# Kernel optimization log

Measured on AMD Instinct MI355X. Metric: run time of the kernel, lower is better.

## Reference

```python
import jax, jax.numpy as jnp
import numpy as np

N, E, L, F, M = 512, 2048, 16, 16, 8
HOPS = 2      # egonet radius (k_hop_subgraph num_hops)
H = 128       # WL hash buckets
N_ITER = 3    # WeisfeilerLehman(n_iter=3)
TAU = 0.1     # soft-relabeling temperature


def setup_inputs():
    key = jax.random.key(0)
    k0, k1, k2, k3, k4, k5 = jax.random.split(key, 6)
    labels = jax.random.randint(k0, (N,), 0, L)
    x = jax.nn.one_hot(labels, L, dtype=jnp.float32)
    edge_index = jax.random.randint(k1, (2, E), 0, N)
    # filter adjacencies, built exactly as in GKernel.__init__:
    # symmetric 0/1 with zero diagonal
    A = jax.random.uniform(k2, (F, M, M))
    A = ((A + jnp.swapaxes(A, -1, -2)) > 1.0).astype(jnp.float32)
    A = A * (1.0 - jnp.eye(M, dtype=jnp.float32))
    Xlab = jax.random.randint(k3, (F, M), 0, L)
    X = jax.nn.one_hot(Xlab, L, dtype=jnp.float32)
    # injective label -> bucket embedding (random distinct buckets)
    E0 = jax.nn.one_hot(jax.random.permutation(k4, H)[:L], H, dtype=jnp.float32)
    # random projection used to hash (own-label, neighbor-multiset) signatures
    Rproj = jax.random.normal(k5, (2 * H, H), dtype=jnp.float32)
    return {"x": x, "edge_index": edge_index, "P": A, "X": X, "E0": E0, "Rproj": Rproj}


def _wl_features(c0, nbr_sum, mask, Rproj):
    # soft Weisfeiler-Lehman subtree features: at each iteration the new
    # node label is a hash of (own label, neighbor-label multiset); the
    # graph feature is the concatenated per-iteration label histograms.
    c = c0 * mask[:, None]                       # [n, H]
    feats = [c.sum(0)]
    for _ in range(N_ITER):
        sig = jnp.concatenate([c, nbr_sum(c)], axis=-1)        # [n, 2H]
        c = jax.nn.softmax((sig @ Rproj) / TAU, axis=-1) * mask[:, None]
        feats.append(c.sum(0))
    return jnp.concatenate(feats)                # [(N_ITER+1)*H]


def _max_comp_mask(A):
    # largest connected component via min-label propagation (max_comp)
    comp = jnp.arange(M, dtype=jnp.float32)
    Ab = A > 0
    for _ in range(M):
        nbr_min = jnp.min(jnp.where(Ab, comp[None, :], 1e9), axis=1)
        comp = jnp.minimum(comp, nbr_min)
    ci = comp.astype(jnp.int32)
    counts = jax.ops.segment_sum(jnp.ones(M, jnp.float32), ci, num_segments=M)
    best = jnp.argmax(counts)
    return (ci == best).astype(jnp.float32)


def reference(x, edge_index, P, X, E0, Rproj):
    # symmetrize edges (egonets / WL kernels are undirected)
    src = jnp.concatenate([edge_index[0], edge_index[1]])
    dst = jnp.concatenate([edge_index[1], edge_index[0]])
    # --- k-hop egonet node masks (compute_egonets) : reach[i, j] = 1 iff
    # node j is within HOPS hops of root i ---
    reach = jnp.eye(N, dtype=jnp.float32)
    for _ in range(HOPS):
        agg = jax.ops.segment_sum(reach[:, src].T, dst, num_segments=N).T
        reach = jnp.clip(reach + agg, 0.0, 1.0)
    c0 = x @ E0                                  # initial bucket labels [N, H]

    def ego_feat(mask):
        emask = (mask[src] * mask[dst])[:, None]
        def nbr(c):
            return jax.ops.segment_sum(c[src] * emask, dst, num_segments=N)
        return _wl_features(c0, nbr, mask, Rproj)

    ego_feats = jax.vmap(ego_feat)(reach)        # [N, (N_ITER+1)*H]

    def filt_feat(Af, Xf):
        mask = _max_comp_mask(Af)
        Am = Af * mask[:, None] * mask[None, :]
        return _wl_features(Xf @ E0, lambda c: Am @ c, mask, Rproj)

    filt_feats = jax.vmap(filt_feat)(P, X)       # [F, (N_ITER+1)*H]

    # normalized WL kernel: k(g1,g2)/sqrt(k(g1,g1) k(g2,g2)); sim.T -> [N, F]
    sim = filt_feats @ ego_feats.T               # [F, N]
    nf = jnp.linalg.norm(filt_feats, axis=-1)
    ng = jnp.linalg.norm(ego_feats, axis=-1)
    sim = sim / (nf[:, None] * ng[None, :] + 1e-12)
    return sim.T
```

## Files before the change

### kernel.cpp

```cpp
#include <hip/hip_runtime.h>
#include <hip/hip_bf16.h>

#define NN 512
#define EE 2048
#define LL 16
#define FF 16
#define MM 8
#define HH 128
#define CAP_ROWS 40960
#define MAXD 32
#define TAU_SCALE 14.426950408889634f

typedef __attribute__((ext_vector_type(8))) short bf16x8;
typedef __attribute__((ext_vector_type(4))) float f32x4;

constexpr size_t OFF_ADJ   = 0;
constexpr size_t SZ_ADJ    = (size_t)NN * 8 * 8;
constexpr size_t OFF_DEG   = OFF_ADJ + SZ_ADJ;
constexpr size_t SZ_DEG    = (size_t)NN * 4;
constexpr size_t OFF_CNT   = OFF_DEG + SZ_DEG;
constexpr size_t SZ_CNT    = (size_t)NN * 4;
constexpr size_t OFF_ROFF  = OFF_CNT + SZ_CNT;
constexpr size_t SZ_ROFF   = (size_t)(NN + 1) * 4 + 12;
constexpr size_t OFF_BUCKN = OFF_ROFF + SZ_ROFF;
constexpr size_t SZ_BUCKN  = (size_t)NN * 4;
constexpr size_t OFF_BUCKF = OFF_BUCKN + SZ_BUCKN;
constexpr size_t SZ_BUCKF  = (size_t)FF * MM * 4;
constexpr size_t OFF_NLST  = ((OFF_BUCKF + SZ_BUCKF + 63) / 64) * 64;
constexpr size_t SZ_NLST   = (size_t)NN * MAXD * 2;
constexpr size_t OFF_CEGO  = OFF_NLST + SZ_NLST;
constexpr size_t SZ_CEGO   = (size_t)CAP_ROWS * 2;
constexpr size_t OFF_NCNT  = OFF_CEGO + SZ_CEGO;
constexpr size_t SZ_NCNT   = (size_t)CAP_ROWS * 2;
constexpr size_t OFF_RBK   = OFF_NCNT + SZ_NCNT;
constexpr size_t SZ_RBK    = (size_t)CAP_ROWS * 2;
constexpr size_t OFF_NBR   = OFF_RBK + SZ_RBK;
constexpr size_t SZ_NBR    = (size_t)CAP_ROWS * MAXD * 2;
constexpr size_t OFF_NBK   = OFF_NBR + SZ_NBR;
constexpr size_t SZ_NBK    = (size_t)CAP_ROWS * MAXD * 2;
constexpr size_t OFF_EGOF  = ((OFF_NBK + SZ_NBK + 63) / 64) * 64;
constexpr size_t SZ_EGOF   = (size_t)NN * 512 * 4;
constexpr size_t OFF_FILTF = OFF_EGOF + SZ_EGOF;
constexpr size_t SZ_FILTF  = (size_t)FF * 512 * 4;
constexpr size_t OFF_FNORM = OFF_FILTF + SZ_FILTF;
constexpr size_t SZ_FNORM  = 64;
constexpr size_t OFF_CA    = ((OFF_FNORM + SZ_FNORM + 255) / 256) * 256;
constexpr size_t SZ_CBUF   = (size_t)CAP_ROWS * HH * 4;
constexpr size_t OFF_CB    = OFF_CA + SZ_CBUF;

__device__ __forceinline__ unsigned f2bfbits(float x) {
    unsigned u = __float_as_uint(x);
    return (u + 0x7fffu + ((u >> 16) & 1u)) >> 16;
}
__device__ __forceinline__ float bf2f(unsigned hb) { return __uint_as_float(hb << 16); }

__global__ __launch_bounds__(256) void k_build(const int* __restrict__ ei,
                                               const float* __restrict__ x,
                                               const float* __restrict__ X,
                                               const float* __restrict__ E0,
                                               int* __restrict__ degN,
                                               unsigned short* __restrict__ nbrLstN,
                                               unsigned long long* __restrict__ adj,
                                               int* __restrict__ buckN,
                                               int* __restrict__ buckF) {
    int idx = blockIdx.x * blockDim.x + threadIdx.x;
    if (idx < EE) {
        int a = ei[idx], b = ei[EE + idx];
        int p = atomicAdd(&degN[a], 1);
        if (p < MAXD) nbrLstN[(size_t)a * MAXD + p] = (unsigned short)b;
        int q = atomicAdd(&degN[b], 1);
        if (q < MAXD) nbrLstN[(size_t)b * MAXD + q] = (unsigned short)a;
        atomicOr(&adj[(size_t)a * 8 + (b >> 6)], 1ull << (b & 63));
        atomicOr(&adj[(size_t)b * 8 + (a >> 6)], 1ull << (a & 63));
    } else if (idx < EE + NN) {
        int i = idx - EE;
        int lab = 0;
        for (int l = 0; l < LL; ++l) if (x[i * LL + l] > 0.5f) lab = l;
        int b = 0;
        for (int h = 0; h < HH; ++h) if (E0[lab * HH + h] > 0.5f) b = h;
        buckN[i] = b;
    } else if (idx < EE + NN + FF * MM) {
        int fm = idx - EE - NN;
        int lab = 0;
        for (int l = 0; l < LL; ++l) if (X[fm * LL + l] > 0.5f) lab = l;
        int b = 0;
        for (int h = 0; h < HH; ++h) if (E0[lab * HH + h] > 0.5f) b = h;
        buckF[fm] = b;
    }
}

__global__ __launch_bounds__(64) void k_reach(const unsigned long long* __restrict__ adj,
                                              unsigned long long* __restrict__ bitsR,
                                              int* __restrict__ count) {
    __shared__ unsigned long long r1[8];
    __shared__ unsigned long long r2[8];
    int i = blockIdx.x, t = threadIdx.x;
    if (t < 8) {
        unsigned long long v = adj[(size_t)i * 8 + t];
        if (t == (i >> 6)) v |= 1ull << (i & 63);
        r1[t] = v;
        r2[t] = v;
    }
    __syncthreads();
    unsigned long long p[8] = {0, 0, 0, 0, 0, 0, 0, 0};
    for (int rep = 0; rep < 8; ++rep) {
        if ((r1[rep] >> t) & 1ull) {
            int j = t + rep * 64;
#pragma unroll
            for (int w = 0; w < 8; ++w) p[w] |= adj[(size_t)j * 8 + w];
        }
    }
#pragma unroll
    for (int w = 0; w < 8; ++w)
        if (p[w]) atomicOr(&r2[w], p[w]);
    __syncthreads();
    if (t < 8) bitsR[(size_t)i * 8 + t] = r2[t];
    if (t == 0) {
        int acc = 0;
        for (int w = 0; w < 8; ++w) acc += __popcll(r2[w]);
        count[i] = acc;
    }
}

__global__ __launch_bounds__(512) void k_scan(const int* __restrict__ in,
                                              int* __restrict__ out) {
    __shared__ int s[NN];
    int t = threadIdx.x;
    s[t] = in[t];
    __syncthreads();
    for (int d = 1; d < NN; d <<= 1) {
        int v = (t >= d) ? s[t - d] : 0;
        __syncthreads();
        s[t] += v;
        __syncthreads();
    }
    out[t + 1] = s[t];
    if (t == 0) out[0] = 0;
}

__global__ __launch_bounds__(64) void k_pack(const unsigned long long* __restrict__ bitsR,
                                             const int* __restrict__ count,
                                             const int* __restrict__ rowOff,
                                             const int* __restrict__ degN,
                                             const unsigned short* __restrict__ nbrLstN,
                                             const int* __restrict__ buckN,
                                             unsigned short* __restrict__ nbrRow,
                                             unsigned short* __restrict__ nbrBuck,
                                             unsigned short* __restrict__ nbrCnt,
                                             unsigned short* __restrict__ rowBuck,
                                             unsigned short* __restrict__ cegoG,
                                             float* __restrict__ egoF) {
    __shared__ unsigned long long bits[8];
    __shared__ int wpre[8];
    __shared__ unsigned short cmap_s[NN];
    __shared__ unsigned short nodes_s[NN];
    __shared__ float f0[HH];
    int i = blockIdx.x, t = threadIdx.x;
    if (t < 8) bits[t] = bitsR[(size_t)i * 8 + t];
    if (t < 64) { f0[t] = 0.0f; f0[t + 64] = 0.0f; }
    __syncthreads();
    if (t == 0) {
        int acc = 0;
        for (int w = 0; w < 8; ++w) { wpre[w] = acc; acc += __popcll(bits[w]); }
    }
    __syncthreads();
    int base = rowOff[i];
    int n = count[i];
    if (base >= CAP_ROWS) n = 0;
    else if (base + n > CAP_ROWS) n = CAP_ROWS - base;
    for (int rep = 0; rep < 8; ++rep) {
        int j = t + rep * 64;
        unsigned long long word = bits[rep];
        unsigned short v = 0xFFFFu;
        if ((word >> t) & 1ull) {
            int idx = wpre[rep] + __popcll(word & ((1ull << t) - 1ull));
            if (idx < n) { v = (unsigned short)idx; nodes_s[idx] = (unsigned short)j; }
        }
        cmap_s[j] = v;
    }
    for (int q = 256 + t; q < 512; q += 64) egoF[(size_t)i * 512 + q] = 0.0f;
    __syncthreads();
    for (int m = t; m < n; m += 64) {
        int j = nodes_s[m];
        int b = buckN[j];
        atomicAdd(&f0[b], 1.0f);
        size_t row = (size_t)(base + m);
        rowBuck[row] = (unsigned short)b;
        int dn = degN[j]; if (dn > MAXD) dn = MAXD;
        int cnt = 0;
        for (int e = 0; e < dn; ++e) {
            unsigned short nbNode = nbrLstN[(size_t)j * MAXD + e];
            unsigned short nr = cmap_s[nbNode];
            if (nr != 0xFFFFu && cnt < MAXD) {
                nbrRow[row * MAXD + cnt] = (unsigned short)(base + nr);
                nbrBuck[row * MAXD + cnt] = (unsigned short)buckN[nbNode];
                cnt++;
            }
        }
        nbrCnt[row] = (unsigned short)cnt;
        cegoG[row] = (unsigned short)i;
    }
    __syncthreads();
    if (t < 64) {
        egoF[(size_t)i * 512 + t] = f0[t];
        egoF[(size_t)i * 512 + t + 64] = f0[t + 64];
    }
}

__global__ __launch_bounds__(256) void k_iter1(const int* __restrict__ count,
                                               const int* __restrict__ rowOff,
                                               const unsigned short* __restrict__ rowBuck,
                                               const unsigned short* __restrict__ nbrBuck,
                                               const unsigned short* __restrict__ nbrCnt,
                                               const float* __restrict__ Rg,
                                               float* __restrict__ cOut,
                                               float* __restrict__ egoF) {
    __shared__ float fs[HH];
    int i = blockIdx.x, tid = threadIdx.x;
    int base = rowOff[i];
    int n = count[i];
    if (base >= CAP_ROWS) n = 0;
    else if (base + n > CAP_ROWS) n = CAP_ROWS - base;
    if (tid < HH) fs[tid] = 0.0f;
    __syncthreads();
    const float* Rb = Rg + (size_t)HH * HH;
    int col = (tid & 7) * 16;
    float facc[16];
#pragma unroll
    for (int q = 0; q < 16; ++q) facc[q] = 0.0f;
    for (int m = tid >> 3; m < n; m += 32) {
        int gr = base + m;
        float z[16];
        const float* rt = Rg + (size_t)rowBuck[gr] * HH + col;
#pragma unroll
        for (int q = 0; q < 4; ++q) *(float4*)&z[q * 4] = *(const float4*)&rt[q * 4];
        int cnt = nbrCnt[gr];
        const unsigned short* nk = &nbrBuck[(size_t)gr * MAXD];
        for (int e = 0; e < cnt; ++e) {
            const float* rb = Rb + (size_t)nk[e] * HH + col;
#pragma unroll
            for (int q = 0; q < 4; ++q) {
                float4 rv = *(const float4*)&rb[q * 4];
                z[q * 4 + 0] += rv.x; z[q * 4 + 1] += rv.y;
                z[q * 4 + 2] += rv.z; z[q * 4 + 3] += rv.w;
            }
        }
        float mx = z[0];
#pragma unroll
        for (int q = 1; q < 16; ++q) mx = fmaxf(mx, z[q]);
        for (int off = 4; off > 0; off >>= 1) mx = fmaxf(mx, __shfl_xor(mx, off));
        float s = 0.0f;
#pragma unroll
        for (int q = 0; q < 16; ++q) { z[q] = exp2f((z[q] - mx) * TAU_SCALE); s += z[q]; }
        for (int off = 4; off > 0; off >>= 1) s += __shfl_xor(s, off);
        float inv = 1.0f / s;
        float* crow = cOut + (size_t)gr * HH + col;
#pragma unroll
        for (int q = 0; q < 16; ++q) { z[q] *= inv; facc[q] += z[q]; }
#pragma unroll
        for (int q = 0; q < 4; ++q) *(float4*)&crow[q * 4] = *(const float4*)&z[q * 4];
    }
#pragma unroll
    for (int q = 0; q < 16; ++q) atomicAdd(&fs[col + q], facc[q]);
    __syncthreads();
    if (tid < HH) egoF[(size_t)i * 512 + HH + tid] = fs[tid];
}

__global__ __launch_bounds__(256) void k_prep(const float* __restrict__ Rg,
                                              short* __restrict__ RtH,
                                              short* __restrict__ RtL) {
    int idx = blockIdx.x * blockDim.x + threadIdx.x;
    int col = idx >> 5;
    int kc = (idx & 31) * 8;
    bf16x8 hv, lv;
#pragma unroll
    for (int j = 0; j < 8; ++j) {
        float xv = Rg[(size_t)(kc + j) * HH + col];
        unsigned hb = f2bfbits(xv);
        hv[j] = (short)hb;
        lv[j] = (short)f2bfbits(xv - bf2f(hb));
    }
    *(bf16x8*)&RtH[(size_t)col * 256 + kc] = hv;
    *(bf16x8*)&RtL[(size_t)col * 256 + kc] = lv;
}

__global__ __launch_bounds__(64) void k_iter(const float* __restrict__ cur,
                                             float* __restrict__ nxt,
                                             const short* __restrict__ RtH,
                                             const short* __restrict__ RtL,
                                             const int* __restrict__ rowOff,
                                             const unsigned short* __restrict__ nbrRow,
                                             const unsigned short* __restrict__ nbrCnt,
                                             const unsigned short* __restrict__ cegoG,
                                             float* __restrict__ egoF,
                                             int it) {
    int Rtot = rowOff[NN];
    if (Rtot > CAP_ROWS) Rtot = CAP_ROWS;
    int r0 = blockIdx.x * 16;
    if (r0 >= Rtot) return;
    int tid = threadIdx.x;
    int c16 = tid & 15, g = tid >> 4;
    int kb = g * 8;
    int grA = r0 + c16;
    if (grA >= Rtot) grA = Rtot - 1;

    float ua[4][8];
#pragma unroll
    for (int s = 0; s < 4; ++s)
#pragma unroll
        for (int j = 0; j < 8; ++j) ua[s][j] = 0.0f;
    {
        int cnt = nbrCnt[grA];
        const unsigned short* nb = &nbrRow[(size_t)grA * MAXD];
        for (int e = 0; e < cnt; ++e) {
            const float* cr = &cur[(size_t)nb[e] * HH + kb];
#pragma unroll
            for (int s = 0; s < 4; ++s) {
                float4 v0 = *(const float4*)&cr[s * 32];
                float4 v1 = *(const float4*)&cr[s * 32 + 4];
                ua[s][0] += v0.x; ua[s][1] += v0.y; ua[s][2] += v0.z; ua[s][3] += v0.w;
                ua[s][4] += v1.x; ua[s][5] += v1.y; ua[s][6] += v1.z; ua[s][7] += v1.w;
            }
        }
    }

    f32x4 acc[8];
#pragma unroll
    for (int n = 0; n < 8; ++n) acc[n] = (f32x4)(0.0f);
    const short* bbH = RtH + (size_t)c16 * 256 + kb;
    const short* bbL = RtL + (size_t)c16 * 256 + kb;

#pragma unroll
    for (int s = 0; s < 4; ++s) {
        bf16x8 ahi, alo;
#pragma unroll
        for (int j = 0; j < 8; ++j) {
            float xv = ua[s][j];
            unsigned hb = f2bfbits(xv);
            ahi[j] = (short)hb;
            alo[j] = (short)f2bfbits(xv - bf2f(hb));
        }
        const int t = s + 4;
#pragma unroll
        for (int n = 0; n < 8; ++n) {
            bf16x8 bh = *(const bf16x8*)&bbH[n * 4096 + t * 32];
            bf16x8 bl = *(const bf16x8*)&bbL[n * 4096 + t * 32];
            acc[n] = __builtin_amdgcn_mfma_f32_16x16x32_bf16(ahi, bh, acc[n], 0, 0, 0);
            acc[n] = __builtin_amdgcn_mfma_f32_16x16x32_bf16(ahi, bl, acc[n], 0, 0, 0);
            acc[n] = __builtin_amdgcn_mfma_f32_16x16x32_bf16(alo, bh, acc[n], 0, 0, 0);
        }
    }
    {
        const float* cr = &cur[(size_t)grA * HH + kb];
#pragma unroll
        for (int t = 0; t < 4; ++t) {
            float4 v0 = *(const float4*)&cr[t * 32];
            float4 v1 = *(const float4*)&cr[t * 32 + 4];
            float cv[8] = {v0.x, v0.y, v0.z, v0.w, v1.x, v1.y, v1.z, v1.w};
            bf16x8 ahi, alo;
#pragma unroll
            for (int j = 0; j < 8; ++j) {
                unsigned hb = f2bfbits(cv[j]);
                ahi[j] = (short)hb;
                alo[j] = (short)f2bfbits(cv[j] - bf2f(hb));
            }
#pragma unroll
            for (int n = 0; n < 8; ++n) {
                bf16x8 bh = *(const bf16x8*)&bbH[n * 4096 + t * 32];
                bf16x8 bl = *(const bf16x8*)&bbL[n * 4096 + t * 32];
                acc[n] = __builtin_amdgcn_mfma_f32_16x16x32_bf16(ahi, bh, acc[n], 0, 0, 0);
                acc[n] = __builtin_amdgcn_mfma_f32_16x16x32_bf16(ahi, bl, acc[n], 0, 0, 0);
                acc[n] = __builtin_amdgcn_mfma_f32_16x16x32_bf16(alo, bh, acc[n], 0, 0, 0);
            }
        }
    }

    float inv[4];
#pragma unroll
    for (int i = 0; i < 4; ++i) {
        float m = acc[0][i];
#pragma unroll
        for (int n = 1; n < 8; ++n) m = fmaxf(m, acc[n][i]);
        for (int off = 8; off > 0; off >>= 1) m = fmaxf(m, __shfl_xor(m, off));
        float s = 0.0f;
#pragma unroll
        for (int n = 0; n < 8; ++n) {
            float e = exp2f((acc[n][i] - m) * TAU_SCALE);
            acc[n][i] = e; s += e;
        }
        for (int off = 8; off > 0; off >>= 1) s += __shfl_xor(s, off);
        inv[i] = 1.0f / s;
    }

    float fa[8];
#pragma unroll
    for (int n = 0; n < 8; ++n) fa[n] = 0.0f;
    int cege = -1;
#pragma unroll
    for (int i = 0; i < 4; ++i) {
        int gr = r0 + g * 4 + i;
        if (gr < Rtot) {
#pragma unroll
            for (int n = 0; n < 8; ++n) {
                float c = acc[n][i] * inv[i];
                nxt[(size_t)gr * HH + n * 16 + c16] = c;
                acc[n][i] = c;
            }
            int ego = cegoG[gr];
            if (ego != cege) {
                if (cege >= 0) {
#pragma unroll
                    for (int n = 0; n < 8; ++n) {
                        atomicAdd(&egoF[(size_t)cege * 512 + it * HH + n * 16 + c16], fa[n]);
                        fa[n] = 0.0f;
                    }
                }
                cege = ego;
            }
#pragma unroll
            for (int n = 0; n < 8; ++n) fa[n] += acc[n][i];
        }
    }
    if (cege >= 0) {
#pragma unroll
        for (int n = 0; n < 8; ++n)
            atomicAdd(&egoF[(size_t)cege * 512 + it * HH + n * 16 + c16], fa[n]);
    }
}

__global__ __launch_bounds__(256) void k_filt(const float* __restrict__ P,
                                              const int* __restrict__ buckF,
                                              const float* __restrict__ Rg,
                                              float* __restrict__ filtF,
                                              float* __restrict__ fnorm) {
    __shared__ float As[MM][MM];
    __shared__ float Am[MM][MM];
    __shared__ float msk[MM];
    __shared__ float cbuf[2][MM][HH];
    __shared__ float ubuf[MM][HH];
    __shared__ float feats[4 * HH];
    __shared__ float red4[4];
    int f = blockIdx.x, tid = threadIdx.x, wave = tid >> 6, lane = tid & 63;
    if (tid < 64) As[tid >> 3][tid & 7] = P[f * 64 + tid];
    for (int idx = tid; idx < 4 * HH; idx += 256) feats[idx] = 0.f;
    __syncthreads();
    if (tid == 0) {
        float comp[MM];
        for (int m = 0; m < MM; ++m) comp[m] = (float)m;
        for (int it = 0; it < MM; ++it) {
            float nm[MM];
            for (int j = 0; j < MM; ++j) {
                float mn = 1e9f;
                for (int k = 0; k < MM; ++k)
                    if (As[j][k] > 0.f) mn = fminf(mn, comp[k]);
                nm[j] = mn;
            }
            for (int j = 0; j < MM; ++j) comp[j] = fminf(comp[j], nm[j]);
        }
        int cnt[MM], ci[MM];
        for (int m = 0; m < MM; ++m) cnt[m] = 0;
        for (int m = 0; m < MM; ++m) { ci[m] = (int)comp[m]; cnt[ci[m]]++; }
        int best = 0;
        for (int m = 1; m < MM; ++m) if (cnt[m] > cnt[best]) best = m;
        for (int m = 0; m < MM; ++m) msk[m] = (ci[m] == best) ? 1.0f : 0.0f;
    }
    __syncthreads();
    if (tid < 64) Am[tid >> 3][tid & 7] = As[tid >> 3][tid & 7] * msk[tid >> 3] * msk[tid & 7];
    for (int idx = tid; idx < MM * HH; idx += 256) {
        int m = idx >> 7, h = idx & 127;
        cbuf[0][m][h] = (msk[m] > 0.f && h == buckF[f * MM + m]) ? 1.0f : 0.0f;
    }
    __syncthreads();
    if (tid < HH) {
        float s = 0.f;
        for (int m = 0; m < MM; ++m) s += cbuf[0][m][tid];
        feats[tid] = s;
    }
    __syncthreads();
    int cur = 0;
    int h2 = 2 * lane;
    for (int it = 1; it <= 3; ++it) {
#pragma unroll
        for (int jj = 0; jj < 2; ++jj) {
            int d = wave * 2 + jj;
            float u0 = 0.f, u1 = 0.f;
            for (int s = 0; s < MM; ++s) {
                float w = Am[d][s];
                u0 += w * cbuf[cur][s][h2];
                u1 += w * cbuf[cur][s][h2 + 1];
            }
            ubuf[d][h2] = u0;
            ubuf[d][h2 + 1] = u1;
        }
        float a0[2] = {0.f, 0.f}, a1[2] = {0.f, 0.f};
        for (int k = 0; k < HH; ++k) {
            float2 rt = *(const float2*)&Rg[(size_t)k * HH + h2];
            float2 rb = *(const float2*)&Rg[(size_t)(HH + k) * HH + h2];
#pragma unroll
            for (int jj = 0; jj < 2; ++jj) {
                int d = wave * 2 + jj;
                float cd = cbuf[cur][d][k];
                float ud = ubuf[d][k];
                a0[jj] += cd * rt.x + ud * rb.x;
                a1[jj] += cd * rt.y + ud * rb.y;
            }
        }
#pragma unroll
        for (int jj = 0; jj < 2; ++jj) {
            int d = wave * 2 + jj;
            float z0 = a0[jj], z1 = a1[jj];
            float m = fmaxf(z0, z1);
            for (int off = 32; off > 0; off >>= 1) m = fmaxf(m, __shfl_xor(m, off));
            float e0 = exp2f((z0 - m) * TAU_SCALE);
            float e1 = exp2f((z1 - m) * TAU_SCALE);
            float s = e0 + e1;
            for (int off = 32; off > 0; off >>= 1) s += __shfl_xor(s, off);
            float inv = msk[d] / s;
            float c0 = e0 * inv, c1 = e1 * inv;
            cbuf[1 - cur][d][h2] = c0;
            cbuf[1 - cur][d][h2 + 1] = c1;
            atomicAdd(&feats[it * HH + h2], c0);
            atomicAdd(&feats[it * HH + h2 + 1], c1);
        }
        __syncthreads();
        cur = 1 - cur;
    }
    float np = 0.f;
    for (int idx = tid; idx < 4 * HH; idx += 256) {
        float v = feats[idx];
        filtF[(size_t)f * 512 + idx] = v;
        np += v * v;
    }
    for (int off = 32; off > 0; off >>= 1) np += __shfl_xor(np, off);
    if (lane == 0) red4[wave] = np;
    __syncthreads();
    if (tid == 0) fnorm[f] = sqrtf(red4[0] + red4[1] + red4[2] + red4[3]);
}

__global__ __launch_bounds__(64) void k_sim(const float* __restrict__ egoF,
                                            const float* __restrict__ filtF,
                                            const float* __restrict__ fnorm,
                                            float* __restrict__ out) {
    int i = blockIdx.x, lane = threadIdx.x;
    float e[8];
    float ss = 0.f;
#pragma unroll
    for (int r = 0; r < 8; ++r) {
        e[r] = egoF[(size_t)i * 512 + r * 64 + lane];
        ss += e[r] * e[r];
    }
    for (int off = 32; off > 0; off >>= 1) ss += __shfl_xor(ss, off);
    float ng = sqrtf(ss);
    for (int f = 0; f < FF; ++f) {
        float d = 0.f;
#pragma unroll
        for (int r = 0; r < 8; ++r) d += e[r] * filtF[(size_t)f * 512 + r * 64 + lane];
        for (int off = 32; off > 0; off >>= 1) d += __shfl_xor(d, off);
        if (lane == 0) out[i * FF + f] = d / (fnorm[f] * ng + 1e-12f);
    }
}

extern "C" void kernel_launch(void* const* d_in, const int* in_sizes, int n_in,
                              void* d_out, int out_size, void* d_ws, size_t ws_size,
                              hipStream_t stream) {
    (void)in_sizes; (void)n_in; (void)out_size; (void)ws_size;
    const float* x  = (const float*)d_in[0];
    const int*   ei = (const int*)d_in[1];
    const float* P  = (const float*)d_in[2];
    const float* X  = (const float*)d_in[3];
    const float* E0 = (const float*)d_in[4];
    const float* Rg = (const float*)d_in[5];
    float* out = (float*)d_out;
    char* ws = (char*)d_ws;

    unsigned long long* adj   = (unsigned long long*)(ws + OFF_ADJ);
    int* degN   = (int*)(ws + OFF_DEG);
    int* count  = (int*)(ws + OFF_CNT);
    int* rowOff = (int*)(ws + OFF_ROFF);
    int* buckN  = (int*)(ws + OFF_BUCKN);
    int* buckF  = (int*)(ws + OFF_BUCKF);
    unsigned short* nbrLstN = (unsigned short*)(ws + OFF_NLST);
    unsigned short* cego    = (unsigned short*)(ws + OFF_CEGO);
    unsigned short* nbrCnt  = (unsigned short*)(ws + OFF_NCNT);
    unsigned short* rowBuck = (unsigned short*)(ws + OFF_RBK);
    unsigned short* nbrRow  = (unsigned short*)(ws + OFF_NBR);
    unsigned short* nbrBuck = (unsigned short*)(ws + OFF_NBK);
    float* egoF  = (float*)(ws + OFF_EGOF);
    float* filtF = (float*)(ws + OFF_FILTF);
    float* fnorm = (float*)(ws + OFF_FNORM);
    float* cA    = (float*)(ws + OFF_CA);
    float* cB    = (float*)(ws + OFF_CB);
    unsigned long long* bitsR = (unsigned long long*)(ws + OFF_CA);
    short* RtH = (short*)(ws + OFF_NBK);
    short* RtL = RtH + (size_t)HH * 256;

    hipMemsetAsync(ws, 0, OFF_CNT, stream);
    k_build<<<(EE + NN + FF * MM + 255) / 256, 256, 0, stream>>>(ei, x, X, E0, degN, nbrLstN,
                                                                 adj, buckN, buckF);
    k_reach<<<NN, 64, 0, stream>>>(adj, bitsR, count);
    k_scan<<<1, 512, 0, stream>>>(count, rowOff);
    k_pack<<<NN, 64, 0, stream>>>(bitsR, count, rowOff, degN, nbrLstN, buckN,
                                  nbrRow, nbrBuck, nbrCnt, rowBuck, cego, egoF);
    k_iter1<<<NN, 256, 0, stream>>>(count, rowOff, rowBuck, nbrBuck, nbrCnt, Rg, cB, egoF);
    k_prep<<<16, 256, 0, stream>>>(Rg, RtH, RtL);
    k_iter<<<CAP_ROWS / 16, 64, 0, stream>>>(cB, cA, RtH, RtL, rowOff, nbrRow, nbrCnt, cego, egoF, 2);
    k_iter<<<CAP_ROWS / 16, 64, 0, stream>>>(cA, cB, RtH, RtL, rowOff, nbrRow, nbrCnt, cego, egoF, 3);
    k_filt<<<FF, 256, 0, stream>>>(P, buckF, Rg, filtF, fnorm);
    k_sim<<<NN, 64, 0, stream>>>(egoF, filtF, fnorm, out);
}
```

Before: 305.7 us.

## Fuse all WL iterations per egonet into one LDS-resident kernel for small egonets

Adds a k_fused kernel that runs the three soft WL iterations for one egonet per block, keeping the per-node label buffers in swizzled shared memory (up to 144 rows) rather than round-tripping through global memory across separate k_iter1/k_iter launches. Large egonets still go through the existing k_iter1/k_iter path, which now skips rows belonging to small egonets. k_prep moves earlier and RtH/RtL get their own workspace region. The intent is to cut global traffic and atomics. In exchange it uses roughly 147 KB of LDS per block, limiting occupancy to one block per CU, and adds per-row block-wide syncs in the softmax.

```diff
diff --git a/kernel.cpp b/kernel.cpp
--- a/kernel.cpp
+++ b/kernel.cpp
@@ -9,6 +9,7 @@
 #define HH 128
 #define CAP_ROWS 40960
 #define MAXD 32
+#define CAPR 144
 #define TAU_SCALE 14.426950408889634f
 
 typedef __attribute__((ext_vector_type(8))) short bf16x8;
@@ -47,6 +48,7 @@
 constexpr size_t OFF_CA    = ((OFF_FNORM + SZ_FNORM + 255) / 256) * 256;
 constexpr size_t SZ_CBUF   = (size_t)CAP_ROWS * HH * 4;
 constexpr size_t OFF_CB    = OFF_CA + SZ_CBUF;
+constexpr size_t OFF_RT    = OFF_CB + SZ_CBUF;
 
 __device__ __forceinline__ unsigned f2bfbits(float x) {
     unsigned u = __float_as_uint(x);
@@ -207,6 +209,337 @@
     }
 }
 
+__global__ __launch_bounds__(256) void k_prep(const float* __restrict__ Rg,
+                                              short* __restrict__ RtH,
+                                              short* __restrict__ RtL) {
+    int idx = blockIdx.x * blockDim.x + threadIdx.x;
+    int col = idx >> 5;
+    int kc = (idx & 31) * 8;
+    bf16x8 hv, lv;
+#pragma unroll
+    for (int j = 0; j < 8; ++j) {
+        float xv = Rg[(size_t)(kc + j) * HH + col];
+        unsigned hb = f2bfbits(xv);
+        hv[j] = (short)hb;
+        lv[j] = (short)f2bfbits(xv - bf2f(hb));
+    }
+    *(bf16x8*)&RtH[(size_t)col * 256 + kc] = hv;
+    *(bf16x8*)&RtL[(size_t)col * 256 + kc] = lv;
+}
+
+__global__ __launch_bounds__(512, 1) void k_fused(const int* __restrict__ count,
+                                                  const int* __restrict__ rowOff,
+                                                  const unsigned short* __restrict__ rowBuck,
+                                                  const unsigned short* __restrict__ nbrBuck,
+                                                  const unsigned short* __restrict__ nbrCnt,
+                                                  const unsigned short* __restrict__ nbrRow,
+                                                  const float* __restrict__ Rg,
+                                                  const short* __restrict__ RtH,
+                                                  const short* __restrict__ RtL,
+                                                  float* __restrict__ egoF) {
+    __shared__ __align__(16) char cAp[CAPR * 512];
+    __shared__ __align__(16) char cBp[CAPR * 512];
+    __shared__ float fs[HH];
+    __shared__ float smax[8][16];
+    __shared__ float ssum[8][16];
+    int ego = blockIdx.x;
+    int n = count[ego];
+    if (n > CAPR) return;
+    int base = rowOff[ego];
+    if (base >= CAP_ROWS) return;
+    if (base + n > CAP_ROWS) n = CAP_ROWS - base;
+    if (n < 1) return;
+    int T = (n + 15) >> 4;
+    int tid = threadIdx.x;
+    int wid = tid >> 6, lane = tid & 63;
+    int c16 = lane & 15, g = lane >> 4, kb = g * 8;
+    int slot = tid >> 3, colg = tid & 7;
+
+    if (tid < HH) fs[tid] = 0.0f;
+    {
+        int padN = (T * 16 - n) * 128;
+        for (int idx = tid; idx < padN; idx += 512) {
+            int r = n + (idx >> 7), h = idx & 127;
+            unsigned b = ((unsigned)(r * 512 + h * 4)) ^ ((unsigned)((r & 7) << 4));
+            *(float*)(cAp + b) = 0.0f;
+            *(float*)(cBp + b) = 0.0f;
+        }
+    }
+    __syncthreads();
+
+    {
+        const float* Rb = Rg + (size_t)HH * HH;
+        float facc[16];
+#pragma unroll
+        for (int q = 0; q < 16; ++q) facc[q] = 0.0f;
+        for (int m = slot; m < n; m += 64) {
+            int gr = base + m;
+            float z[16];
+            const float* rt = Rg + (size_t)rowBuck[gr] * HH + colg * 16;
+#pragma unroll
+            for (int q = 0; q < 4; ++q) *(float4*)&z[q * 4] = *(const float4*)&rt[q * 4];
+            int cnt = nbrCnt[gr];
+            const unsigned short* nk = &nbrBuck[(size_t)gr * MAXD];
+            for (int e = 0; e < cnt; ++e) {
+                const float* rb = Rb + (size_t)nk[e] * HH + colg * 16;
+#pragma unroll
+                for (int q = 0; q < 4; ++q) {
+                    float4 rv = *(const float4*)&rb[q * 4];
+                    z[q * 4 + 0] += rv.x; z[q * 4 + 1] += rv.y;
+                    z[q * 4 + 2] += rv.z; z[q * 4 + 3] += rv.w;
+                }
+            }
+            float mx = z[0];
+#pragma unroll
+            for (int q = 1; q < 16; ++q) mx = fmaxf(mx, z[q]);
+            for (int off = 4; off > 0; off >>= 1) mx = fmaxf(mx, __shfl_xor(mx, off));
+            float s = 0.0f;
+#pragma unroll
+            for (int q = 0; q < 16; ++q) { z[q] = exp2f((z[q] - mx) * TAU_SCALE); s += z[q]; }
+            for (int off = 4; off > 0; off >>= 1) s += __shfl_xor(s, off);
+            float inv = 1.0f / s;
+#pragma unroll
+            for (int q = 0; q < 16; ++q) { z[q] *= inv; facc[q] += z[q]; }
+            unsigned swr = (unsigned)((m & 7) << 4);
+#pragma unroll
+            for (int q = 0; q < 4; ++q) {
+                unsigned b = ((unsigned)(m * 512 + colg * 64 + q * 16)) ^ swr;
+                *(float4*)(cAp + b) = *(float4*)&z[q * 4];
+            }
+        }
+#pragma unroll
+        for (int q = 0; q < 16; ++q) {
+            float v = facc[q];
+            v += __shfl_xor(v, 8); v += __shfl_xor(v, 16); v += __shfl_xor(v, 32);
+            if (lane < 8) atomicAdd(&fs[lane * 16 + q], v);
+        }
+    }
+    __syncthreads();
+    if (tid < HH) egoF[(size_t)ego * 512 + HH + tid] = fs[tid];
+
+    bf16x8 bH[8], bL[8];
+    {
+        const short* pH = RtH + (size_t)(wid * 16 + c16) * 256 + kb;
+        const short* pL = RtL + (size_t)(wid * 16 + c16) * 256 + kb;
+#pragma unroll
+        for (int t = 0; t < 8; ++t) {
+            bH[t] = *(const bf16x8*)&pH[t * 32];
+            bL[t] = *(const bf16x8*)&pL[t * 32];
+        }
+    }
+
+    for (int m = slot; m < n; m += 64) {
+        int gr = base + m;
+        float v[16];
+#pragma unroll
+        for (int q = 0; q < 16; ++q) v[q] = 0.0f;
+        int cnt = nbrCnt[gr];
+        const unsigned short* nb = &nbrRow[(size_t)gr * MAXD];
+        for (int e = 0; e < cnt; ++e) {
+            int lr = (int)nb[e] - base;
+            unsigned swr = (unsigned)((lr & 7) << 4);
+#pragma unroll
+            for (int q = 0; q < 4; ++q) {
+                unsigned b = ((unsigned)(lr * 512 + colg * 64 + q * 16)) ^ swr;
+                float4 t4 = *(const float4*)(cAp + b);
+                v[q * 4 + 0] += t4.x; v[q * 4 + 1] += t4.y;
+                v[q * 4 + 2] += t4.z; v[q * 4 + 3] += t4.w;
+            }
+        }
+        unsigned swd = (unsigned)((m & 7) << 4);
+#pragma unroll
+        for (int q = 0; q < 4; ++q) {
+            unsigned b = ((unsigned)(m * 512 + colg * 64 + q * 16)) ^ swd;
+            *(float4*)(cBp + b) = *(float4*)&v[q * 4];
+        }
+    }
+    __syncthreads();
+
+    float facc2 = 0.0f;
+    for (int t = 0; t < T; ++t) {
+        int rowA = 16 * t + c16;
+        unsigned swr = (unsigned)((rowA & 7) << 4);
+        unsigned rbase = (unsigned)rowA * 512u;
+        f32x4 acc = (f32x4)(0.0f);
+#pragma unroll
+        for (int s = 0; s < 4; ++s) {
+            unsigned b0 = (rbase + (unsigned)(s * 128 + g * 32)) ^ swr;
+            float4 v0 = *(const float4*)(cBp + b0);
+            float4 v1 = *(const float4*)(cBp + (b0 ^ 16u));
+            float uv[8] = {v0.x, v0.y, v0.z, v0.w, v1.x, v1.y, v1.z, v1.w};
+            bf16x8 ahi, alo;
+#pragma unroll
+            for (int j = 0; j < 8; ++j) {
+                unsigned hb = f2bfbits(uv[j]);
+                ahi[j] = (short)hb;
+                alo[j] = (short)f2bfbits(uv[j] - bf2f(hb));
+            }
+            acc = __builtin_amdgcn_mfma_f32_16x16x32_bf16(ahi, bH[s + 4], acc, 0, 0, 0);
+            acc = __builtin_amdgcn_mfma_f32_16x16x32_bf16(ahi, bL[s + 4], acc, 0, 0, 0);
+            acc = __builtin_amdgcn_mfma_f32_16x16x32_bf16(alo, bH[s + 4], acc, 0, 0, 0);
+        }
+#pragma unroll
+        for (int s = 0; s < 4; ++s) {
+            unsigned b0 = (rbase + (unsigned)(s * 128 + g * 32)) ^ swr;
+            float4 v0 = *(const float4*)(cAp + b0);
+            float4 v1 = *(const float4*)(cAp + (b0 ^ 16u));
+            float cv[8] = {v0.x, v0.y, v0.z, v0.w, v1.x, v1.y, v1.z, v1.w};
+            bf16x8 ahi, alo;
+#pragma unroll
+            for (int j = 0; j < 8; ++j) {
+                unsigned hb = f2bfbits(cv[j]);
+                ahi[j] = (short)hb;
+                alo[j] = (short)f2bfbits(cv[j] - bf2f(hb));
+            }
+            acc = __builtin_amdgcn_mfma_f32_16x16x32_bf16(ahi, bH[s], acc, 0, 0, 0);
+            acc = __builtin_amdgcn_mfma_f32_16x16x32_bf16(ahi, bL[s], acc, 0, 0, 0);
+            acc = __builtin_amdgcn_mfma_f32_16x16x32_bf16(alo, bH[s], acc, 0, 0, 0);
+        }
+#pragma unroll
+        for (int i = 0; i < 4; ++i) {
+            float m = acc[i];
+            for (int off = 8; off > 0; off >>= 1) m = fmaxf(m, __shfl_xor(m, off));
+            if (c16 == 0) smax[wid][4 * g + i] = m;
+        }
+        __syncthreads();
+#pragma unroll
+        for (int i = 0; i < 4; ++i) {
+            int rr = 4 * g + i;
+            float m = smax[0][rr];
+#pragma unroll
+            for (int w2 = 1; w2 < 8; ++w2) m = fmaxf(m, smax[w2][rr]);
+            float e = exp2f((acc[i] - m) * TAU_SCALE);
+            acc[i] = e;
+            float s = e;
+            for (int off = 8; off > 0; off >>= 1) s += __shfl_xor(s, off);
+            if (c16 == 0) ssum[wid][rr] = s;
+        }
+        __syncthreads();
+#pragma unroll
+        for (int i = 0; i < 4; ++i) {
+            int rr = 4 * g + i;
+            float s = ssum[0][rr];
+#pragma unroll
+            for (int w2 = 1; w2 < 8; ++w2) s += ssum[w2][rr];
+            float inv = 1.0f / s;
+            float cv = acc[i] * inv;
+            int row = 16 * t + rr;
+            unsigned b = ((unsigned)(row * 512 + (wid * 16 + c16) * 4)) ^ ((unsigned)((row & 7) << 4));
+            *(float*)(cBp + b) = cv;
+            if (row < n) facc2 += cv;
+        }
+    }
+    __syncthreads();
+    {
+        float v = facc2;
+        v += __shfl_xor(v, 16); v += __shfl_xor(v, 32);
+        if (g == 0) egoF[(size_t)ego * 512 + 2 * HH + wid * 16 + c16] = v;
+    }
+
+    for (int m = slot; m < n; m += 64) {
+        int gr = base + m;
+        float v[16];
+#pragma unroll
+        for (int q = 0; q < 16; ++q) v[q] = 0.0f;
+        int cnt = nbrCnt[gr];
+        const unsigned short* nb = &nbrRow[(size_t)gr * MAXD];
+        for (int e = 0; e < cnt; ++e) {
+            int lr = (int)nb[e] - base;
+            unsigned swr = (unsigned)((lr & 7) << 4);
+#pragma unroll
+            for (int q = 0; q < 4; ++q) {
+                unsigned b = ((unsigned)(lr * 512 + colg * 64 + q * 16)) ^ swr;
+                float4 t4 = *(const float4*)(cBp + b);
+                v[q * 4 + 0] += t4.x; v[q * 4 + 1] += t4.y;
+                v[q * 4 + 2] += t4.z; v[q * 4 + 3] += t4.w;
+            }
+        }
+        unsigned swd = (unsigned)((m & 7) << 4);
+#pragma unroll
+        for (int q = 0; q < 4; ++q) {
+            unsigned b = ((unsigned)(m * 512 + colg * 64 + q * 16)) ^ swd;
+            *(float4*)(cAp + b) = *(float4*)&v[q * 4];
+        }
+    }
+    __syncthreads();
+
+    float facc3 = 0.0f;
+    for (int t = 0; t < T; ++t) {
+        int rowA = 16 * t + c16;
+        unsigned swr = (unsigned)((rowA & 7) << 4);
+        unsigned rbase = (unsigned)rowA * 512u;
+        f32x4 acc = (f32x4)(0.0f);
+#pragma unroll
+        for (int s = 0; s < 4; ++s) {
+            unsigned b0 = (rbase + (unsigned)(s * 128 + g * 32)) ^ swr;
+            float4 v0 = *(const float4*)(cAp + b0);
+            float4 v1 = *(const float4*)(cAp + (b0 ^ 16u));
+            float uv[8] = {v0.x, v0.y, v0.z, v0.w, v1.x, v1.y, v1.z, v1.w};
+            bf16x8 ahi, alo;
+#pragma unroll
+            for (int j = 0; j < 8; ++j) {
+                unsigned hb = f2bfbits(uv[j]);
+                ahi[j] = (short)hb;
+                alo[j] = (short)f2bfbits(uv[j] - bf2f(hb));
+            }
+            acc = __builtin_amdgcn_mfma_f32_16x16x32_bf16(ahi, bH[s + 4], acc, 0, 0, 0);
+            acc = __builtin_amdgcn_mfma_f32_16x16x32_bf16(ahi, bL[s + 4], acc, 0, 0, 0);
+            acc = __builtin_amdgcn_mfma_f32_16x16x32_bf16(alo, bH[s + 4], acc, 0, 0, 0);
+        }
+#pragma unroll
+        for (int s = 0; s < 4; ++s) {
+            unsigned b0 = (rbase + (unsigned)(s * 128 + g * 32)) ^ swr;
+            float4 v0 = *(const float4*)(cBp + b0);
+            float4 v1 = *(const float4*)(cBp + (b0 ^ 16u));
+            float cv[8] = {v0.x, v0.y, v0.z, v0.w, v1.x, v1.y, v1.z, v1.w};
+            bf16x8 ahi, alo;
+#pragma unroll
+            for (int j = 0; j < 8; ++j) {
+                unsigned hb = f2bfbits(cv[j]);
+                ahi[j] = (short)hb;
+                alo[j] = (short)f2bfbits(cv[j] - bf2f(hb));
+            }
+            acc = __builtin_amdgcn_mfma_f32_16x16x32_bf16(ahi, bH[s], acc, 0, 0, 0);
+            acc = __builtin_amdgcn_mfma_f32_16x16x32_bf16(ahi, bL[s], acc, 0, 0, 0);
+            acc = __builtin_amdgcn_mfma_f32_16x16x32_bf16(alo, bH[s], acc, 0, 0, 0);
+        }
+#pragma unroll
+        for (int i = 0; i < 4; ++i) {
+            float m = acc[i];
+            for (int off = 8; off > 0; off >>= 1) m = fmaxf(m, __shfl_xor(m, off));
+            if (c16 == 0) smax[wid][4 * g + i] = m;
+        }
+        __syncthreads();
+#pragma unroll
+        for (int i = 0; i < 4; ++i) {
+            int rr = 4 * g + i;
+            float m = smax[0][rr];
+#pragma unroll
+            for (int w2 = 1; w2 < 8; ++w2) m = fmaxf(m, smax[w2][rr]);
+            float e = exp2f((acc[i] - m) * TAU_SCALE);
+            acc[i] = e;
+            float s = e;
+            for (int off = 8; off > 0; off >>= 1) s += __shfl_xor(s, off);
+            if (c16 == 0) ssum[wid][rr] = s;
+        }
+        __syncthreads();
+#pragma unroll
+        for (int i = 0; i < 4; ++i) {
+            int rr = 4 * g + i;
+            float s = ssum[0][rr];
+#pragma unroll
+            for (int w2 = 1; w2 < 8; ++w2) s += ssum[w2][rr];
+            int row = 16 * t + rr;
+            if (row < n) facc3 += acc[i] * (1.0f / s);
+        }
+    }
+    {
+        float v = facc3;
+        v += __shfl_xor(v, 16); v += __shfl_xor(v, 32);
+        if (g == 0) egoF[(size_t)ego * 512 + 3 * HH + wid * 16 + c16] = v;
+    }
+}
+
 __global__ __launch_bounds__(256) void k_iter1(const int* __restrict__ count,
                                                const int* __restrict__ rowOff,
                                                const unsigned short* __restrict__ rowBuck,
@@ -217,6 +550,7 @@
                                                float* __restrict__ egoF) {
     __shared__ float fs[HH];
     int i = blockIdx.x, tid = threadIdx.x;
+    if (count[i] <= CAPR) return;
     int base = rowOff[i];
     int n = count[i];
     if (base >= CAP_ROWS) n = 0;
@@ -266,29 +600,12 @@
     if (tid < HH) egoF[(size_t)i * 512 + HH + tid] = fs[tid];
 }
 
-__global__ __launch_bounds__(256) void k_prep(const float* __restrict__ Rg,
-                                              short* __restrict__ RtH,
-                                              short* __restrict__ RtL) {
-    int idx = blockIdx.x * blockDim.x + threadIdx.x;
-    int col = idx >> 5;
-    int kc = (idx & 31) * 8;
-    bf16x8 hv, lv;
-#pragma unroll
-    for (int j = 0; j < 8; ++j) {
-        float xv = Rg[(size_t)(kc + j) * HH + col];
-        unsigned hb = f2bfbits(xv);
-        hv[j] = (short)hb;
-        lv[j] = (short)f2bfbits(xv - bf2f(hb));
-    }
-    *(bf16x8*)&RtH[(size_t)col * 256 + kc] = hv;
-    *(bf16x8*)&RtL[(size_t)col * 256 + kc] = lv;
-}
-
 __global__ __launch_bounds__(64) void k_iter(const float* __restrict__ cur,
                                              float* __restrict__ nxt,
                                              const short* __restrict__ RtH,
                                              const short* __restrict__ RtL,
                                              const int* __restrict__ rowOff,
+                                             const int* __restrict__ count,
                                              const unsigned short* __restrict__ nbrRow,
                                              const unsigned short* __restrict__ nbrCnt,
                                              const unsigned short* __restrict__ cegoG,
@@ -303,6 +620,8 @@
     int kb = g * 8;
     int grA = r0 + c16;
     if (grA >= Rtot) grA = Rtot - 1;
+    bool bigA = count[cegoG[grA]] > CAPR;
+    if (__ballot(bigA) == 0ull) return;
 
     float ua[4][8];
 #pragma unroll
@@ -310,7 +629,7 @@
 #pragma unroll
         for (int j = 0; j < 8; ++j) ua[s][j] = 0.0f;
     {
-        int cnt = nbrCnt[grA];
+        int cnt = bigA ? (int)nbrCnt[grA] : 0;
         const unsigned short* nb = &nbrRow[(size_t)grA * MAXD];
         for (int e = 0; e < cnt; ++e) {
             const float* cr = &cur[(size_t)nb[e] * HH + kb];
@@ -323,13 +642,11 @@
             }
         }
     }
-
     f32x4 acc[8];
 #pragma unroll
     for (int n = 0; n < 8; ++n) acc[n] = (f32x4)(0.0f);
     const short* bbH = RtH + (size_t)c16 * 256 + kb;
     const short* bbL = RtL + (size_t)c16 * 256 + kb;
-
 #pragma unroll
     for (int s = 0; s < 4; ++s) {
         bf16x8 ahi, alo;
@@ -374,7 +691,6 @@
             }
         }
     }
-
     float inv[4];
 #pragma unroll
     for (int i = 0; i < 4; ++i) {
@@ -391,7 +707,6 @@
         for (int off = 8; off > 0; off >>= 1) s += __shfl_xor(s, off);
         inv[i] = 1.0f / s;
     }
-
     float fa[8];
 #pragma unroll
     for (int n = 0; n < 8; ++n) fa[n] = 0.0f;
@@ -400,25 +715,27 @@
     for (int i = 0; i < 4; ++i) {
         int gr = r0 + g * 4 + i;
         if (gr < Rtot) {
-#pragma unroll
-            for (int n = 0; n < 8; ++n) {
-                float c = acc[n][i] * inv[i];
-                nxt[(size_t)gr * HH + n * 16 + c16] = c;
-                acc[n][i] = c;
-            }
             int ego = cegoG[gr];
-            if (ego != cege) {
-                if (cege >= 0) {
-#pragma unroll
-                    for (int n = 0; n < 8; ++n) {
-                        atomicAdd(&egoF[(size_t)cege * 512 + it * HH + n * 16 + c16], fa[n]);
-                        fa[n] = 0.0f;
+            if (count[ego] > CAPR) {
+#pragma unroll
+                for (int n = 0; n < 8; ++n) {
+                    float c = acc[n][i] * inv[i];
+                    nxt[(size_t)gr * HH + n * 16 + c16] = c;
+                    acc[n][i] = c;
+                }
+                if (ego != cege) {
+                    if (cege >= 0) {
+#pragma unroll
+                        for (int n = 0; n < 8; ++n) {
+                            atomicAdd(&egoF[(size_t)cege * 512 + it * HH + n * 16 + c16], fa[n]);
+                            fa[n] = 0.0f;
+                        }
                     }
+                    cege = ego;
                 }
-                cege = ego;
-            }
-#pragma unroll
-            for (int n = 0; n < 8; ++n) fa[n] += acc[n][i];
+#pragma unroll
+                for (int n = 0; n < 8; ++n) fa[n] += acc[n][i];
+            }
         }
     }
     if (cege >= 0) {
@@ -591,20 +908,22 @@
     float* cA    = (float*)(ws + OFF_CA);
     float* cB    = (float*)(ws + OFF_CB);
     unsigned long long* bitsR = (unsigned long long*)(ws + OFF_CA);
-    short* RtH = (short*)(ws + OFF_NBK);
+    short* RtH = (short*)(ws + OFF_RT);
     short* RtL = RtH + (size_t)HH * 256;
 
     hipMemsetAsync(ws, 0, OFF_CNT, stream);
     k_build<<<(EE + NN + FF * MM + 255) / 256, 256, 0, stream>>>(ei, x, X, E0, degN, nbrLstN,
                                                                  adj, buckN, buckF);
+    k_prep<<<16, 256, 0, stream>>>(Rg, RtH, RtL);
     k_reach<<<NN, 64, 0, stream>>>(adj, bitsR, count);
     k_scan<<<1, 512, 0, stream>>>(count, rowOff);
     k_pack<<<NN, 64, 0, stream>>>(bitsR, count, rowOff, degN, nbrLstN, buckN,
                                   nbrRow, nbrBuck, nbrCnt, rowBuck, cego, egoF);
+    k_fused<<<NN, 512, 0, stream>>>(count, rowOff, rowBuck, nbrBuck, nbrCnt, nbrRow,
+                                    Rg, RtH, RtL, egoF);
     k_iter1<<<NN, 256, 0, stream>>>(count, rowOff, rowBuck, nbrBuck, nbrCnt, Rg, cB, egoF);
-    k_prep<<<16, 256, 0, stream>>>(Rg, RtH, RtL);
-    k_iter<<<CAP_ROWS / 16, 64, 0, stream>>>(cB, cA, RtH, RtL, rowOff, nbrRow, nbrCnt, cego, egoF, 2);
-    k_iter<<<CAP_ROWS / 16, 64, 0, stream>>>(cA, cB, RtH, RtL, rowOff, nbrRow, nbrCnt, cego, egoF, 3);
+    k_iter<<<CAP_ROWS / 16, 64, 0, stream>>>(cB, cA, RtH, RtL, rowOff, count, nbrRow, nbrCnt, cego, egoF, 2);
+    k_iter<<<CAP_ROWS / 16, 64, 0, stream>>>(cA, cB, RtH, RtL, rowOff, count, nbrRow, nbrCnt, cego, egoF, 3);
     k_filt<<<FF, 256, 0, stream>>>(P, buckF, Rg, filtF, fnorm);
     k_sim<<<NN, 64, 0, stream>>>(egoF, filtF, fnorm, out);
 }
```

Result: slower. 319.0 us (+4.3%).
